# Optimization experiments

Hardware: AMD Instinct MI355X
Metric: run time of the kernel (lower is better)

The kernel has to match this reference:

```python
import jax, jax.numpy as jnp
import numpy as np

N = 50000          # nodes
F = 128            # feature dim (indim = outdim)
AVG_DEG = 12       # random edges per node (plus one self-loop)
AVG_D_LOG = 2.6    # avg_d['log'] used by PNA scalers
EPS = 1e-5         # PNA std epsilon / BatchNorm eps


def setup_inputs() -> dict:
    key = jax.random.key(0)
    k1, k2, k3, k4 = jax.random.split(key, 4)
    h = jax.random.normal(k1, (N, F), dtype=jnp.float32)
    E_rand = N * AVG_DEG
    src_r = jax.random.randint(k2, (E_rand,), 0, N)
    dst_r = jax.random.randint(k3, (E_rand,), 0, N)
    loop = jnp.arange(N)
    src = jnp.concatenate([src_r, loop]).astype(jnp.int64) if jax.config.jax_enable_x64 else jnp.concatenate([src_r, loop]).astype(jnp.int32)
    dst = jnp.concatenate([dst_r, loop]).astype(src.dtype)
    concat_dim = F * (1 + 4 * 3)  # indim * (1 + n_aggr * n_scalers)
    W = jax.random.normal(k4, (concat_dim, F), dtype=jnp.float32) * (1.0 / np.sqrt(concat_dim))
    b = jnp.zeros((F,), dtype=jnp.float32)
    gamma = jnp.ones((F,), dtype=jnp.float32)
    beta = jnp.zeros((F,), dtype=jnp.float32)
    return {"h": h, "src": src, "dst": dst, "W": W, "b": b, "gamma": gamma, "beta": beta}


def _pna_forward(h, W, b, gamma, beta, src, dst):
    n = h.shape[0]
    m = h[src]                                            # [E, F] gathered mailbox
    deg = jax.ops.segment_sum(jnp.ones(src.shape[0], h.dtype), dst, num_segments=n)
    deg = jnp.maximum(deg, 1.0)[:, None]                  # every node has a self-loop
    s = jax.ops.segment_sum(m, dst, num_segments=n)
    mean = s / deg
    mx = jax.ops.segment_max(m, dst, num_segments=n)
    mn = jax.ops.segment_min(m, dst, num_segments=n)
    mean_sq = jax.ops.segment_sum(m * m, dst, num_segments=n) / deg
    std = jnp.sqrt(jax.nn.relu(mean_sq - mean * mean) + EPS)
    agg = jnp.concatenate([mean, mx, mn, std], axis=1)    # [N, 4F]
    logd = jnp.log(deg + 1.0)                             # [N, 1]
    scaled = jnp.concatenate([agg,
                              agg * (logd / AVG_D_LOG),
                              agg * (AVG_D_LOG / logd)], axis=1)  # [N, 12F]
    hc = jnp.concatenate([h, scaled], axis=1)             # [N, 13F]
    out = hc @ W + b                                      # posttrans (single linear)
    out = jax.nn.relu(out)                                # activation (dropout p=0)
    mu = out.mean(axis=0)                                 # BatchNorm1d, training stats
    var = out.var(axis=0)                                 # biased variance (torch)
    out = gamma * (out - mu) * jax.lax.rsqrt(var + EPS) + beta
    return out


def reference(h, src, dst, W, b, gamma, beta):
    return _pna_forward(h, W, b, gamma, beta, src, dst)
```

## Files before the change

### kernel.cpp

```cpp
#include <hip/hip_runtime.h>
#include <math.h>

#define FDIM 128
#define AVG_D_LOGF 2.6f
#define BN_EPS 1e-5f
#define NK 10

using f32x2 = __attribute__((ext_vector_type(2))) float;
using f32x4 = __attribute__((ext_vector_type(4))) float;
using s16x8 = __attribute__((ext_vector_type(8))) short;
using u16x8 = __attribute__((ext_vector_type(8))) unsigned short;

__device__ __forceinline__ unsigned short f2bf(float x) {
  unsigned int u = __float_as_uint(x);
  u += 0x7FFFu + ((u >> 16) & 1u);
  return (unsigned short)(u >> 16);
}
__device__ __forceinline__ float bf2f(unsigned short u) {
  return __uint_as_float(((unsigned int)u) << 16);
}
__device__ __forceinline__ f32x2 bfpair(unsigned int u) {
  union { uint2 u2; f32x2 f; } c;
  c.u2 = make_uint2(u << 16, u & 0xFFFF0000u);
  return c.f;
}

__device__ __forceinline__ void gload16(const void* g, void* l) {
  __builtin_amdgcn_global_load_lds(
      (const __attribute__((address_space(1))) void*)g,
      (__attribute__((address_space(3))) void*)l, 16, 0, 0);
}

__global__ void prep_kernel(const float* __restrict__ h, unsigned short* __restrict__ hb,
                            const float* __restrict__ W, unsigned short* __restrict__ wBT,
                            const int* __restrict__ dst, int* __restrict__ deg,
                            int w0, int w1, int w2, int K) {
  int i = blockIdx.x * 256 + threadIdx.x;
  if (i < w0) {
    const f32x4* sp = (const f32x4*)h + (size_t)i * 2;
    f32x4 v0 = sp[0], v1 = sp[1];
    u16x8 o;
    o[0] = f2bf(v0[0]); o[1] = f2bf(v0[1]); o[2] = f2bf(v0[2]); o[3] = f2bf(v0[3]);
    o[4] = f2bf(v1[0]); o[5] = f2bf(v1[1]); o[6] = f2bf(v1[2]); o[7] = f2bf(v1[3]);
    *((u16x8*)hb + i) = o;
  } else if (i < w0 + w1) {
    int idx = i - w0;
    int k = idx >> 7, j = idx & 127;
    wBT[(size_t)j * K + k] = f2bf(W[idx]);
  } else if (i < w0 + w1 + w2) {
    atomicAdd(&deg[dst[i - w0 - w1]], 1);
  }
}

__global__ void scan1(const int* __restrict__ deg, int* __restrict__ offs,
                      int* __restrict__ bsums, int n) {
  __shared__ int tmp[256];
  int t = threadIdx.x, i = blockIdx.x * 256 + t;
  int v = (i < n) ? deg[i] : 0;
  tmp[t] = v; __syncthreads();
  for (int d = 1; d < 256; d <<= 1) {
    int x = (t >= d) ? tmp[t - d] : 0;
    __syncthreads();
    tmp[t] += x;
    __syncthreads();
  }
  if (i < n) offs[i] = tmp[t] - v;
  if (t == 255) bsums[blockIdx.x] = tmp[255];
}

__global__ void csr_fill(const int* __restrict__ src, const int* __restrict__ dst,
                         const int* __restrict__ offs, const int* __restrict__ bsums,
                         int* __restrict__ cursor, int* __restrict__ csr, int E, int nb) {
  __shared__ int tmp[256];
  __shared__ int ex[256];
  const int t = threadIdx.x;
  {
    int v = (t < nb) ? bsums[t] : 0;
    tmp[t] = v; __syncthreads();
    for (int d = 1; d < 256; d <<= 1) {
      int x = (t >= d) ? tmp[t - d] : 0;
      __syncthreads();
      tmp[t] += x;
      __syncthreads();
    }
    ex[t] = tmp[t] - v;
    __syncthreads();
  }
  int i = blockIdx.x * 256 + t;
  if (i < E) {
    int d = dst[i];
    int pos = offs[d] + ex[d >> 8] + atomicAdd(&cursor[d], 1);
    csr[pos] = src[i] << 8;
  }
}

__global__ __launch_bounds__(256) void agg_kernel(
    const unsigned short* __restrict__ hb, const int* __restrict__ csr,
    const int* __restrict__ offs, const int* __restrict__ bsums,
    unsigned short* __restrict__ aggb, float2* __restrict__ s12a,
    int n, int E, int nb) {
  __shared__ int tmp[256];
  __shared__ int ex[256];
  {
    int t = threadIdx.x;
    int v = (t < nb) ? bsums[t] : 0;
    tmp[t] = v; __syncthreads();
    for (int d = 1; d < 256; d <<= 1) {
      int x = (t >= d) ? tmp[t - d] : 0;
      __syncthreads();
      tmp[t] += x;
      __syncthreads();
    }
    ex[t] = tmp[t] - v;
    __syncthreads();
  }
  const int gw = (blockIdx.x * 256 + threadIdx.x) >> 6;
  const int lane = threadIdx.x & 63;
  if (gw >= n) return;
  const int beg = offs[gw] + ex[gw >> 8];
  const int end = (gw + 1 < n) ? offs[gw + 1] + ex[(gw + 1) >> 8] : E;
  const int sub = lane >> 5;
  const int fl  = lane & 31;
  const char* hbase = (const char*)hb + fl * 8;

  f32x2 s0v = {0.f, 0.f}, s1v = {0.f, 0.f};
  f32x2 q0v = {0.f, 0.f}, q1v = {0.f, 0.f};
  f32x2 mx0 = {-INFINITY, -INFINITY}, mx1 = {-INFINITY, -INFINITY};
  f32x2 mn0 = {INFINITY, INFINITY},  mn1 = {INFINITY, INFINITY};

  auto acc1 = [&](uint2 A) {
    f32x2 a0 = bfpair(A.x), a1 = bfpair(A.y);
    asm("v_pk_add_f32 %0, %0, %1" : "+v"(s0v) : "v"(a0));
    asm("v_pk_add_f32 %0, %0, %1" : "+v"(s1v) : "v"(a1));
    asm("v_pk_fma_f32 %0, %1, %1, %0" : "+v"(q0v) : "v"(a0));
    asm("v_pk_fma_f32 %0, %1, %1, %0" : "+v"(q1v) : "v"(a1));
    mx0[0] = fmaxf(mx0[0], a0[0]); mx0[1] = fmaxf(mx0[1], a0[1]);
    mx1[0] = fmaxf(mx1[0], a1[0]); mx1[1] = fmaxf(mx1[1], a1[1]);
    mn0[0] = fminf(mn0[0], a0[0]); mn0[1] = fminf(mn0[1], a0[1]);
    mn1[0] = fminf(mn1[0], a1[0]); mn1[1] = fminf(mn1[1], a1[1]);
  };
  auto gat = [&](int byteoff) -> uint2 {
    return *(const uint2*)(hbase + byteoff);
  };

  const int cnt = end - beg;
  const int pairs = cnt >> 1;
  int p = 0;
  for (; p + 4 <= pairs; p += 4) {
    int base = beg + 2 * p + sub;
    int i0 = csr[base], i1 = csr[base + 2], i2 = csr[base + 4], i3 = csr[base + 6];
    uint2 A = gat(i0), B = gat(i1), C = gat(i2), D = gat(i3);
    acc1(A); acc1(B); acc1(C); acc1(D);
  }
  for (; p < pairs; ++p) {
    acc1(gat(csr[beg + 2 * p + sub]));
  }
  if ((cnt & 1) && sub == 0) {
    acc1(gat(csr[end - 1]));
  }

  s0v[0] += __shfl_xor(s0v[0], 32); s0v[1] += __shfl_xor(s0v[1], 32);
  s1v[0] += __shfl_xor(s1v[0], 32); s1v[1] += __shfl_xor(s1v[1], 32);
  q0v[0] += __shfl_xor(q0v[0], 32); q0v[1] += __shfl_xor(q0v[1], 32);
  q1v[0] += __shfl_xor(q1v[0], 32); q1v[1] += __shfl_xor(q1v[1], 32);
  mx0[0] = fmaxf(mx0[0], __shfl_xor(mx0[0], 32)); mx0[1] = fmaxf(mx0[1], __shfl_xor(mx0[1], 32));
  mx1[0] = fmaxf(mx1[0], __shfl_xor(mx1[0], 32)); mx1[1] = fmaxf(mx1[1], __shfl_xor(mx1[1], 32));
  mn0[0] = fminf(mn0[0], __shfl_xor(mn0[0], 32)); mn0[1] = fminf(mn0[1], __shfl_xor(mn0[1], 32));
  mn1[0] = fminf(mn1[0], __shfl_xor(mn1[0], 32)); mn1[1] = fminf(mn1[1], __shfl_xor(mn1[1], 32));

  float degf = (float)cnt;
  if (degf < 1.f) degf = 1.f;
  const float inv = 1.f / degf;
  if (sub == 0) {
    float me0 = s0v[0] * inv, me1 = s0v[1] * inv, me2 = s1v[0] * inv, me3 = s1v[1] * inv;
    float st0 = sqrtf(fmaxf(q0v[0] * inv - me0 * me0, 0.f) + BN_EPS);
    float st1 = sqrtf(fmaxf(q0v[1] * inv - me1 * me1, 0.f) + BN_EPS);
    float st2 = sqrtf(fmaxf(q1v[0] * inv - me2 * me2, 0.f) + BN_EPS);
    float st3 = sqrtf(fmaxf(q1v[1] * inv - me3 * me3, 0.f) + BN_EPS);
    unsigned int b = (unsigned int)gw * 512u + (unsigned int)fl * 4u;
    uint2 wme = make_uint2((unsigned int)f2bf(me0) | ((unsigned int)f2bf(me1) << 16),
                           (unsigned int)f2bf(me2) | ((unsigned int)f2bf(me3) << 16));
    uint2 wmx = make_uint2((unsigned int)f2bf(mx0[0]) | ((unsigned int)f2bf(mx0[1]) << 16),
                           (unsigned int)f2bf(mx1[0]) | ((unsigned int)f2bf(mx1[1]) << 16));
    uint2 wmn = make_uint2((unsigned int)f2bf(mn0[0]) | ((unsigned int)f2bf(mn0[1]) << 16),
                           (unsigned int)f2bf(mn1[0]) | ((unsigned int)f2bf(mn1[1]) << 16));
    uint2 wst = make_uint2((unsigned int)f2bf(st0) | ((unsigned int)f2bf(st1) << 16),
                           (unsigned int)f2bf(st2) | ((unsigned int)f2bf(st3) << 16));
    *(uint2*)&aggb[b      ] = wme;
    *(uint2*)&aggb[b + 128] = wmx;
    *(uint2*)&aggb[b + 256] = wmn;
    *(uint2*)&aggb[b + 384] = wst;
  }
  if (lane == 0) {
    float logd = logf(degf + 1.f);
    s12a[gw] = make_float2(logd / AVG_D_LOGF, AVG_D_LOGF / logd);
  }
}

__global__ __launch_bounds__(256, 2) void gemm_kernel(
    const unsigned short* __restrict__ hb, const unsigned short* __restrict__ wBT,
    const unsigned short* __restrict__ aggb, const float2* __restrict__ s12a,
    const float* __restrict__ bias, float* __restrict__ out,
    float* __restrict__ bnsum, float* __restrict__ bnsq, int n, int K) {
  __shared__ s16x8 AsB[2][1024];
  __shared__ s16x8 BsB[2][3][512];
  const int t = threadIdx.x;
  const int lane = t & 63;
  const int w = t >> 6;
  const int wr = w >> 1, wc = w & 1;
  const int hi = lane >> 4, lr = lane & 15, rx7 = lr & 7;

  const int nwg = gridDim.x;
  const int q = nwg >> 3, r = nwg & 7;
  const int xcd = blockIdx.x & 7, jj = blockIdx.x >> 3;
  const int bx = (xcd < r ? xcd * (q + 1) : r * (q + 1) + (xcd - r) * q) + jj;

  const int m0 = (bx >> 1) * 128;
  const int n0 = (bx & 1) * 64;

  f32x4 acc[3][4][2] = {};

  auto stage = [&](int ss, int buf) {
    const bool ph1 = (ss < 2);
    #pragma unroll
    for (int i = 0; i < 4; ++i) {
      int unit = w * 256 + i * 64 + lane;
      int row = unit >> 3, x = unit & 7;
      int node = m0 + row; if (node >= n) node = n - 1;
      int xo = (x ^ (row & 7)) << 3;
      const unsigned short* src = ph1
          ? hb   + (size_t)node * FDIM + ss * 64 + xo
          : aggb + (size_t)node * 512 + (ss - 2) * 64 + xo;
      gload16(src, &AsB[buf][w * 256 + i * 64]);
    }
    const int nsec = ph1 ? 1 : 3;
    for (int s = 0; s < nsec; ++s) {
      int koff = ph1 ? ss * 64 : (FDIM + s * 512 + (ss - 2) * 64);
      #pragma unroll
      for (int i = 0; i < 2; ++i) {
        int unit = w * 128 + i * 64 + lane;
        int row = unit >> 3, x = unit & 7;
        const unsigned short* src =
            wBT + (size_t)(n0 + row) * K + koff + ((x ^ (row & 7)) << 3);
        gload16(src, &BsB[buf][s][w * 128 + i * 64]);
      }
    }
  };

  stage(0, 0);
  int cur = 0;
  for (int step = 0; step < NK; ++step) {
    if (step + 1 < NK) {
      stage(step + 1, cur ^ 1);
      if (step + 1 < 2) asm volatile("s_waitcnt vmcnt(6)" ::: "memory");
      else              asm volatile("s_waitcnt vmcnt(10)" ::: "memory");
    } else {
      asm volatile("s_waitcnt vmcnt(0)" ::: "memory");
    }
    asm volatile("s_barrier" ::: "memory");
    #pragma unroll
    for (int ks = 0; ks < 2; ++ks) {
      s16x8 a[4];
      #pragma unroll
      for (int m = 0; m < 4; ++m) {
        int row = wr * 64 + m * 16 + lr;
        a[m] = AsB[cur][row * 8 + ((ks * 4 + hi) ^ rx7)];
      }
      #pragma unroll
      for (int s = 0; s < 3; ++s) {
        if (step < 2 && s > 0) continue;
        int rb = wc * 32 + lr;
        s16x8 b0 = BsB[cur][s][rb * 8 + ((ks * 4 + hi) ^ rx7)];
        s16x8 b1 = BsB[cur][s][(rb + 16) * 8 + ((ks * 4 + hi) ^ rx7)];
        #pragma unroll
        for (int m = 0; m < 4; ++m) {
          acc[s][m][0] = __builtin_amdgcn_mfma_f32_16x16x32_bf16(a[m], b0, acc[s][m][0], 0, 0, 0);
          acc[s][m][1] = __builtin_amdgcn_mfma_f32_16x16x32_bf16(a[m], b1, acc[s][m][1], 0, 0, 0);
        }
      }
    }
    asm volatile("s_barrier" ::: "memory");
    cur ^= 1;
  }

  float* red = (float*)&AsB[0][0];
  if (t < 128) red[t] = 0.f;
  __syncthreads();

  const float bv0 = bias[n0 + wc * 32 + lr];
  const float bv1 = bias[n0 + wc * 32 + 16 + lr];
  float cs[2] = {0.f, 0.f}, cq[2] = {0.f, 0.f};
  #pragma unroll
  for (int m = 0; m < 4; ++m) {
    #pragma unroll
    for (int i = 0; i < 4; ++i) {
      int grow = m0 + wr * 64 + m * 16 + hi * 4 + i;
      if (grow >= n) continue;
      float2 sv = s12a[grow];
      #pragma unroll
      for (int nn = 0; nn < 2; ++nn) {
        float v = acc[0][m][nn][i] + sv.x * acc[1][m][nn][i] + sv.y * acc[2][m][nn][i]
                + (nn ? bv1 : bv0);
        v = fmaxf(v, 0.f);
        out[(size_t)grow * FDIM + n0 + wc * 32 + nn * 16 + lr] = v;
        cs[nn] += v; cq[nn] += v * v;
      }
    }
  }
  #pragma unroll
  for (int nn = 0; nn < 2; ++nn) {
    int lc = wc * 32 + nn * 16 + lr;
    atomicAdd(&red[lc], cs[nn]);
    atomicAdd(&red[64 + lc], cq[nn]);
  }
  __syncthreads();
  if (t < 64)       atomicAdd(&bnsum[n0 + t], red[t]);
  else if (t < 128) atomicAdd(&bnsq[n0 + t - 64], red[t]);
}

__global__ void bn_norm(float* __restrict__ out, const float* __restrict__ bnsum,
                        const float* __restrict__ bnsq, const float* __restrict__ gamma,
                        const float* __restrict__ beta, int n) {
  __shared__ float scs[128], shs[128];
  const int t = threadIdx.x;
  if (t < 128) {
    const float invN = 1.f / (float)n;
    const float mu = bnsum[t] * invN;
    const float var = bnsq[t] * invN - mu * mu;
    const float rs = rsqrtf(var + BN_EPS);
    const float s = gamma[t] * rs;
    scs[t] = s; shs[t] = beta[t] - mu * s;
  }
  __syncthreads();
  const int total = n * 32;
  int idx = blockIdx.x * 256 + t;
  const int c4 = (idx & 31) * 4;
  const float s0 = scs[c4], s1 = scs[c4 + 1], s2 = scs[c4 + 2], s3 = scs[c4 + 3];
  const float h0 = shs[c4], h1 = shs[c4 + 1], h2 = shs[c4 + 2], h3 = shs[c4 + 3];
  for (; idx < total; idx += gridDim.x * 256) {
    f32x4 v = ((f32x4*)out)[idx];
    v[0] = v[0] * s0 + h0;
    v[1] = v[1] * s1 + h1;
    v[2] = v[2] * s2 + h2;
    v[3] = v[3] * s3 + h3;
    ((f32x4*)out)[idx] = v;
  }
}

extern "C" void kernel_launch(void* const* d_in, const int* in_sizes, int n_in,
                              void* d_out, int out_size, void* d_ws, size_t ws_size,
                              hipStream_t stream) {
  const float* h     = (const float*)d_in[0];
  const int*   src   = (const int*)d_in[1];
  const int*   dst   = (const int*)d_in[2];
  const float* W     = (const float*)d_in[3];
  const float* bias  = (const float*)d_in[4];
  const float* gamma = (const float*)d_in[5];
  const float* beta  = (const float*)d_in[6];
  float* out = (float*)d_out;

  const int n = in_sizes[0] / FDIM;
  const int E = in_sizes[1];
  const int K = in_sizes[3] / FDIM;

  char* base = (char*)d_ws;
  size_t off = 0;
  auto alloc = [&](size_t bytes) -> void* {
    void* p = base + off;
    off += (bytes + 255) & ~(size_t)255;
    return p;
  };
  int*   deg    = (int*)  alloc(4ull * n);
  int*   cursor = (int*)  alloc(4ull * n);
  float* bnsum  = (float*)alloc(512);
  float* bnsq   = (float*)alloc(512);
  const size_t zlen = off;
  int*    offs  = (int*)  alloc(4ull * (n + 1));
  int*    bsums = (int*)  alloc(4ull * 256);
  int*    csr   = (int*)  alloc(4ull * E);
  float2* s12a  = (float2*)alloc(8ull * n);
  unsigned short* aggb = (unsigned short*)alloc(2ull * (size_t)n * 512);
  unsigned short* wBT  = (unsigned short*)alloc(2ull * (size_t)K * FDIM);
  unsigned short* hb   = (unsigned short*)alloc(2ull * (size_t)n * FDIM);
  (void)ws_size; (void)n_in; (void)out_size;

  const int eb = (E + 255) / 256;
  const int nb = (n + 255) / 256;
  const int w0 = n * FDIM / 8;
  const int w1 = K * FDIM;
  const int w2 = E;

  hipMemsetAsync(d_ws, 0, zlen, stream);
  prep_kernel<<<(w0 + w1 + w2 + 255) / 256, 256, 0, stream>>>(h, hb, W, wBT, dst, deg,
                                                              w0, w1, w2, K);
  scan1<<<nb, 256, 0, stream>>>(deg, offs, bsums, n);
  csr_fill<<<eb, 256, 0, stream>>>(src, dst, offs, bsums, cursor, csr, E, nb);
  agg_kernel<<<(n + 3) / 4, 256, 0, stream>>>(hb, csr, offs, bsums, aggb, s12a, n, E, nb);
  const int gblocks = ((n + 127) / 128) * 2;
  gemm_kernel<<<gblocks, 256, 0, stream>>>(hb, wBT, aggb, s12a, bias,
                                           out, bnsum, bnsq, n, K);
  bn_norm<<<2048, 256, 0, stream>>>(out, bnsum, bnsq, gamma, beta, n);
}
```

Measured before the change: 175.1 us.

## Replace double-buffered K=64 GEMM pipeline with single-buffered K=128 steps

The GEMM main loop now stages 128-wide K slices in five steps instead of 64-wide slices in ten. It drops the double buffer and the manual vmcnt waits in favour of __syncthreads, so global-to-LDS loads no longer overlap MFMA work. Fewer iterations and barriers are traded for lost load/compute overlap, with LDS size unchanged. The aggregation kernel's inline-asm packed add/fma is also replaced with plain vector arithmetic, leaving instruction choice to the compiler.

```diff
diff --git a/kernel.cpp b/kernel.cpp
--- a/kernel.cpp
+++ b/kernel.cpp
@@ -4,7 +4,7 @@
 #define FDIM 128
 #define AVG_D_LOGF 2.6f
 #define BN_EPS 1e-5f
-#define NK 10
+#define NK5 5
 
 using f32x2 = __attribute__((ext_vector_type(2))) float;
 using f32x4 = __attribute__((ext_vector_type(4))) float;
@@ -16,15 +16,11 @@
   u += 0x7FFFu + ((u >> 16) & 1u);
   return (unsigned short)(u >> 16);
 }
-__device__ __forceinline__ float bf2f(unsigned short u) {
-  return __uint_as_float(((unsigned int)u) << 16);
-}
 __device__ __forceinline__ f32x2 bfpair(unsigned int u) {
   union { uint2 u2; f32x2 f; } c;
   c.u2 = make_uint2(u << 16, u & 0xFFFF0000u);
   return c.f;
 }
-
 __device__ __forceinline__ void gload16(const void* g, void* l) {
   __builtin_amdgcn_global_load_lds(
       (const __attribute__((address_space(1))) void*)g,
@@ -130,10 +126,8 @@
 
   auto acc1 = [&](uint2 A) {
     f32x2 a0 = bfpair(A.x), a1 = bfpair(A.y);
-    asm("v_pk_add_f32 %0, %0, %1" : "+v"(s0v) : "v"(a0));
-    asm("v_pk_add_f32 %0, %0, %1" : "+v"(s1v) : "v"(a1));
-    asm("v_pk_fma_f32 %0, %1, %1, %0" : "+v"(q0v) : "v"(a0));
-    asm("v_pk_fma_f32 %0, %1, %1, %0" : "+v"(q1v) : "v"(a1));
+    s0v += a0; s1v += a1;
+    q0v += a0 * a0; q1v += a1 * a1;
     mx0[0] = fmaxf(mx0[0], a0[0]); mx0[1] = fmaxf(mx0[1], a0[1]);
     mx1[0] = fmaxf(mx1[0], a1[0]); mx1[1] = fmaxf(mx1[1], a1[1]);
     mn0[0] = fminf(mn0[0], a0[0]); mn0[1] = fminf(mn0[1], a0[1]);
@@ -202,8 +196,8 @@
     const unsigned short* __restrict__ aggb, const float2* __restrict__ s12a,
     const float* __restrict__ bias, float* __restrict__ out,
     float* __restrict__ bnsum, float* __restrict__ bnsq, int n, int K) {
-  __shared__ s16x8 AsB[2][1024];
-  __shared__ s16x8 BsB[2][3][512];
+  __shared__ s16x8 As[2048];
+  __shared__ s16x8 Bs[3][1024];
   const int t = threadIdx.x;
   const int lane = t & 63;
   const int w = t >> 6;
@@ -220,58 +214,53 @@
 
   f32x4 acc[3][4][2] = {};
 
-  auto stage = [&](int ss, int buf) {
-    const bool ph1 = (ss < 2);
+  auto stage = [&](int ss) {
+    const bool ph1 = (ss == 0);
     #pragma unroll
-    for (int i = 0; i < 4; ++i) {
-      int unit = w * 256 + i * 64 + lane;
-      int row = unit >> 3, x = unit & 7;
+    for (int i = 0; i < 8; ++i) {
+      int unit = w * 512 + i * 64 + lane;
+      int row = unit >> 4, xf = unit & 15;
+      int half = xf >> 3, x = xf & 7;
       int node = m0 + row; if (node >= n) node = n - 1;
-      int xo = (x ^ (row & 7)) << 3;
+      int col = half * 64 + ((x ^ (row & 7)) << 3);
       const unsigned short* src = ph1
-          ? hb   + (size_t)node * FDIM + ss * 64 + xo
-          : aggb + (size_t)node * 512 + (ss - 2) * 64 + xo;
-      gload16(src, &AsB[buf][w * 256 + i * 64]);
+          ? hb   + (size_t)node * FDIM + col
+          : aggb + (size_t)node * 512 + (ss - 1) * 128 + col;
+      gload16(src, &As[w * 512 + i * 64]);
     }
     const int nsec = ph1 ? 1 : 3;
     for (int s = 0; s < nsec; ++s) {
-      int koff = ph1 ? ss * 64 : (FDIM + s * 512 + (ss - 2) * 64);
+      int koff = ph1 ? 0 : (FDIM + s * 512 + (ss - 1) * 128);
       #pragma unroll
-      for (int i = 0; i < 2; ++i) {
-        int unit = w * 128 + i * 64 + lane;
-        int row = unit >> 3, x = unit & 7;
-        const unsigned short* src =
-            wBT + (size_t)(n0 + row) * K + koff + ((x ^ (row & 7)) << 3);
-        gload16(src, &BsB[buf][s][w * 128 + i * 64]);
+      for (int i = 0; i < 4; ++i) {
+        int unit = w * 256 + i * 64 + lane;
+        int row = unit >> 4, xf = unit & 15;
+        int half = xf >> 3, x = xf & 7;
+        int col = half * 64 + ((x ^ (row & 7)) << 3);
+        const unsigned short* src = wBT + (size_t)(n0 + row) * K + koff + col;
+        gload16(src, &Bs[s][w * 256 + i * 64]);
       }
     }
   };
 
-  stage(0, 0);
-  int cur = 0;
-  for (int step = 0; step < NK; ++step) {
-    if (step + 1 < NK) {
-      stage(step + 1, cur ^ 1);
-      if (step + 1 < 2) asm volatile("s_waitcnt vmcnt(6)" ::: "memory");
-      else              asm volatile("s_waitcnt vmcnt(10)" ::: "memory");
-    } else {
-      asm volatile("s_waitcnt vmcnt(0)" ::: "memory");
-    }
-    asm volatile("s_barrier" ::: "memory");
+  for (int step = 0; step < NK5; ++step) {
+    stage(step);
+    __syncthreads();
     #pragma unroll
-    for (int ks = 0; ks < 2; ++ks) {
+    for (int ks = 0; ks < 4; ++ks) {
+      const int uidx = ((ks >> 1) << 3) + ((((ks << 2) + hi) & 7) ^ rx7);
       s16x8 a[4];
       #pragma unroll
       for (int m = 0; m < 4; ++m) {
         int row = wr * 64 + m * 16 + lr;
-        a[m] = AsB[cur][row * 8 + ((ks * 4 + hi) ^ rx7)];
+        a[m] = As[row * 16 + uidx];
       }
       #pragma unroll
       for (int s = 0; s < 3; ++s) {
-        if (step < 2 && s > 0) continue;
+        if (step == 0 && s > 0) continue;
         int rb = wc * 32 + lr;
-        s16x8 b0 = BsB[cur][s][rb * 8 + ((ks * 4 + hi) ^ rx7)];
-        s16x8 b1 = BsB[cur][s][(rb + 16) * 8 + ((ks * 4 + hi) ^ rx7)];
+        s16x8 b0 = Bs[s][rb * 16 + uidx];
+        s16x8 b1 = Bs[s][(rb + 16) * 16 + uidx];
         #pragma unroll
         for (int m = 0; m < 4; ++m) {
           acc[s][m][0] = __builtin_amdgcn_mfma_f32_16x16x32_bf16(a[m], b0, acc[s][m][0], 0, 0, 0);
@@ -279,11 +268,10 @@
         }
       }
     }
-    asm volatile("s_barrier" ::: "memory");
-    cur ^= 1;
-  }
-
-  float* red = (float*)&AsB[0][0];
+    __syncthreads();
+  }
+
+  float* red = (float*)&As[0];
   if (t < 128) red[t] = 0.f;
   __syncthreads();
 
```

Result: no change. 174.5 us (-0.3%).

## Prefetch aggregate A-tiles through registers two stages ahead in GEMM loop

Applied to the files above, without the earlier changes.

Restructures the fused GEMM main loop. The two h-phase steps now run unpipelined with direct LDS loads. The aggregate-phase A tiles are loaded into registers two k-steps ahead and written to LDS after compute, while B tiles still use async global-to-LDS loads one step ahead. Address computation is hoisted out of the staging lambdas, and the loop is fully unrolled with hand-tuned vmcnt waits. This aims to hide more global-load latency for the large aggregate operand, at the cost of extra registers, fragile manual waitcount bookkeeping and a non-overlapped first phase. The aggregation kernel's inline-asm packed ops are also replaced with plain vector arithmetic.

```diff
diff --git a/kernel.cpp b/kernel.cpp
--- a/kernel.cpp
+++ b/kernel.cpp
@@ -4,7 +4,6 @@
 #define FDIM 128
 #define AVG_D_LOGF 2.6f
 #define BN_EPS 1e-5f
-#define NK 10
 
 using f32x2 = __attribute__((ext_vector_type(2))) float;
 using f32x4 = __attribute__((ext_vector_type(4))) float;
@@ -16,15 +15,11 @@
   u += 0x7FFFu + ((u >> 16) & 1u);
   return (unsigned short)(u >> 16);
 }
-__device__ __forceinline__ float bf2f(unsigned short u) {
-  return __uint_as_float(((unsigned int)u) << 16);
-}
 __device__ __forceinline__ f32x2 bfpair(unsigned int u) {
   union { uint2 u2; f32x2 f; } c;
   c.u2 = make_uint2(u << 16, u & 0xFFFF0000u);
   return c.f;
 }
-
 __device__ __forceinline__ void gload16(const void* g, void* l) {
   __builtin_amdgcn_global_load_lds(
       (const __attribute__((address_space(1))) void*)g,
@@ -130,10 +125,8 @@
 
   auto acc1 = [&](uint2 A) {
     f32x2 a0 = bfpair(A.x), a1 = bfpair(A.y);
-    asm("v_pk_add_f32 %0, %0, %1" : "+v"(s0v) : "v"(a0));
-    asm("v_pk_add_f32 %0, %0, %1" : "+v"(s1v) : "v"(a1));
-    asm("v_pk_fma_f32 %0, %1, %1, %0" : "+v"(q0v) : "v"(a0));
-    asm("v_pk_fma_f32 %0, %1, %1, %0" : "+v"(q1v) : "v"(a1));
+    s0v += a0; s1v += a1;
+    q0v += a0 * a0; q1v += a1 * a1;
     mx0[0] = fmaxf(mx0[0], a0[0]); mx0[1] = fmaxf(mx0[1], a0[1]);
     mx1[0] = fmaxf(mx1[0], a1[0]); mx1[1] = fmaxf(mx1[1], a1[1]);
     mn0[0] = fminf(mn0[0], a0[0]); mn0[1] = fminf(mn0[1], a0[1]);
@@ -152,12 +145,8 @@
     uint2 A = gat(i0), B = gat(i1), C = gat(i2), D = gat(i3);
     acc1(A); acc1(B); acc1(C); acc1(D);
   }
-  for (; p < pairs; ++p) {
-    acc1(gat(csr[beg + 2 * p + sub]));
-  }
-  if ((cnt & 1) && sub == 0) {
-    acc1(gat(csr[end - 1]));
-  }
+  for (; p < pairs; ++p) acc1(gat(csr[beg + 2 * p + sub]));
+  if ((cnt & 1) && sub == 0) acc1(gat(csr[end - 1]));
 
   s0v[0] += __shfl_xor(s0v[0], 32); s0v[1] += __shfl_xor(s0v[1], 32);
   s1v[0] += __shfl_xor(s1v[0], 32); s1v[1] += __shfl_xor(s1v[1], 32);
@@ -220,52 +209,53 @@
 
   f32x4 acc[3][4][2] = {};
 
-  auto stage = [&](int ss, int buf) {
+  const unsigned short* aH[4];
+  const unsigned short* aG[4];
+  #pragma unroll
+  for (int i = 0; i < 4; ++i) {
+    int unit = w * 256 + i * 64 + lane;
+    int row = unit >> 3, x = unit & 7;
+    int node = m0 + row; if (node >= n) node = n - 1;
+    int col = (x ^ (row & 7)) << 3;
+    aH[i] = hb   + (size_t)node * FDIM + col;
+    aG[i] = aggb + (size_t)node * 512  + col;
+  }
+  const unsigned short* bB[2];
+  #pragma unroll
+  for (int i = 0; i < 2; ++i) {
+    int unit = w * 128 + i * 64 + lane;
+    int row = unit >> 3, x = unit & 7;
+    bB[i] = wBT + (size_t)(n0 + row) * K + ((x ^ (row & 7)) << 3);
+  }
+
+  auto stageB = [&](int ss, int buf) {
     const bool ph1 = (ss < 2);
-    #pragma unroll
-    for (int i = 0; i < 4; ++i) {
-      int unit = w * 256 + i * 64 + lane;
-      int row = unit >> 3, x = unit & 7;
-      int node = m0 + row; if (node >= n) node = n - 1;
-      int xo = (x ^ (row & 7)) << 3;
-      const unsigned short* src = ph1
-          ? hb   + (size_t)node * FDIM + ss * 64 + xo
-          : aggb + (size_t)node * 512 + (ss - 2) * 64 + xo;
-      gload16(src, &AsB[buf][w * 256 + i * 64]);
-    }
     const int nsec = ph1 ? 1 : 3;
     for (int s = 0; s < nsec; ++s) {
       int koff = ph1 ? ss * 64 : (FDIM + s * 512 + (ss - 2) * 64);
       #pragma unroll
-      for (int i = 0; i < 2; ++i) {
-        int unit = w * 128 + i * 64 + lane;
-        int row = unit >> 3, x = unit & 7;
-        const unsigned short* src =
-            wBT + (size_t)(n0 + row) * K + koff + ((x ^ (row & 7)) << 3);
-        gload16(src, &BsB[buf][s][w * 128 + i * 64]);
-      }
-    }
-  };
-
-  stage(0, 0);
-  int cur = 0;
-  for (int step = 0; step < NK; ++step) {
-    if (step + 1 < NK) {
-      stage(step + 1, cur ^ 1);
-      if (step + 1 < 2) asm volatile("s_waitcnt vmcnt(6)" ::: "memory");
-      else              asm volatile("s_waitcnt vmcnt(10)" ::: "memory");
-    } else {
-      asm volatile("s_waitcnt vmcnt(0)" ::: "memory");
-    }
-    asm volatile("s_barrier" ::: "memory");
+      for (int i = 0; i < 2; ++i)
+        gload16(bB[i] + koff, &BsB[buf][s][w * 128 + i * 64]);
+    }
+  };
+  s16x8 rA[4], rA2[4];
+  auto loadA = [&](int ss, s16x8* rr) {
+    #pragma unroll
+    for (int i = 0; i < 4; ++i)
+      rr[i] = *(const s16x8*)(aG[i] + (ss - 2) * 64);
+  };
+  auto writeA = [&](const s16x8* rr, int buf) {
+    #pragma unroll
+    for (int i = 0; i < 4; ++i)
+      AsB[buf][w * 256 + i * 64 + lane] = rr[i];
+  };
+  auto compute = [&](int step, int cur) {
     #pragma unroll
     for (int ks = 0; ks < 2; ++ks) {
       s16x8 a[4];
       #pragma unroll
-      for (int m = 0; m < 4; ++m) {
-        int row = wr * 64 + m * 16 + lr;
-        a[m] = AsB[cur][row * 8 + ((ks * 4 + hi) ^ rx7)];
-      }
+      for (int m = 0; m < 4; ++m)
+        a[m] = AsB[cur][(wr * 64 + m * 16 + lr) * 8 + ((ks * 4 + hi) ^ rx7)];
       #pragma unroll
       for (int s = 0; s < 3; ++s) {
         if (step < 2 && s > 0) continue;
@@ -279,11 +269,52 @@
         }
       }
     }
-    asm volatile("s_barrier" ::: "memory");
-    cur ^= 1;
+  };
+
+  #pragma unroll
+  for (int ss = 0; ss < 2; ++ss) {
+    #pragma unroll
+    for (int i = 0; i < 4; ++i)
+      gload16(aH[i] + ss * 64, &AsB[ss][w * 256 + i * 64]);
+    stageB(ss, ss);
+    __syncthreads();
+    compute(0, ss);
+    __syncthreads();
+  }
+
+  stageB(2, 0);
+  asm volatile("" ::: "memory");
+  loadA(2, rA);
+  asm volatile("s_waitcnt vmcnt(0)" ::: "memory");
+  writeA(rA, 0);
+  loadA(3, rA);
+  asm volatile("s_waitcnt lgkmcnt(0)" ::: "memory");
+  __builtin_amdgcn_s_barrier();
+
+  #pragma unroll
+  for (int tt = 2; tt <= 9; ++tt) {
+    const int p = tt & 1;
+    if (tt <= 8) {
+      stageB(tt + 1, p ^ 1);
+      asm volatile("" ::: "memory");
+    }
+    if (tt <= 7) loadA(tt + 2, rA2);
+    compute(2, p);
+    if (tt <= 8) {
+      if (tt <= 7) asm volatile("s_waitcnt vmcnt(10)" ::: "memory");
+      else         asm volatile("s_waitcnt vmcnt(6)"  ::: "memory");
+      writeA(rA, p ^ 1);
+      #pragma unroll
+      for (int i = 0; i < 4; ++i) rA[i] = rA2[i];
+      if (tt <= 7) asm volatile("s_waitcnt vmcnt(4)" ::: "memory");
+      else         asm volatile("s_waitcnt vmcnt(0)" ::: "memory");
+      asm volatile("s_waitcnt lgkmcnt(0)" ::: "memory");
+      __builtin_amdgcn_s_barrier();
+    }
   }
 
   float* red = (float*)&AsB[0][0];
+  __syncthreads();
   if (t < 128) red[t] = 0.f;
   __syncthreads();
 
```

Result: no change. 177.3 us (+1.3%).

## Shrink GEMM M-tile to 64 rows, drop double buffering, raise occupancy

Applied to the files above, without the earlier changes.

The GEMM block tile is halved from 128 to 64 rows, so the grid doubles and each wave holds half as many accumulators. The double-buffered async LDS pipeline with manual vmcnt waits is replaced by a single buffer loaded then synchronized with __syncthreads, and launch bounds are raised to allow 4 blocks per CU. The agg kernel's inline-asm packed add/fma is replaced with vector-type arithmetic the compiler may lower equivalently. The aim is more blocks in flight to hide latency, at the cost of losing intra-block load/compute overlap and more redundant B-tile loads.

```diff
diff --git a/kernel.cpp b/kernel.cpp
--- a/kernel.cpp
+++ b/kernel.cpp
@@ -16,15 +16,11 @@
   u += 0x7FFFu + ((u >> 16) & 1u);
   return (unsigned short)(u >> 16);
 }
-__device__ __forceinline__ float bf2f(unsigned short u) {
-  return __uint_as_float(((unsigned int)u) << 16);
-}
 __device__ __forceinline__ f32x2 bfpair(unsigned int u) {
   union { uint2 u2; f32x2 f; } c;
   c.u2 = make_uint2(u << 16, u & 0xFFFF0000u);
   return c.f;
 }
-
 __device__ __forceinline__ void gload16(const void* g, void* l) {
   __builtin_amdgcn_global_load_lds(
       (const __attribute__((address_space(1))) void*)g,
@@ -130,10 +126,8 @@
 
   auto acc1 = [&](uint2 A) {
     f32x2 a0 = bfpair(A.x), a1 = bfpair(A.y);
-    asm("v_pk_add_f32 %0, %0, %1" : "+v"(s0v) : "v"(a0));
-    asm("v_pk_add_f32 %0, %0, %1" : "+v"(s1v) : "v"(a1));
-    asm("v_pk_fma_f32 %0, %1, %1, %0" : "+v"(q0v) : "v"(a0));
-    asm("v_pk_fma_f32 %0, %1, %1, %0" : "+v"(q1v) : "v"(a1));
+    s0v += a0; s1v += a1;
+    q0v += a0 * a0; q1v += a1 * a1;
     mx0[0] = fmaxf(mx0[0], a0[0]); mx0[1] = fmaxf(mx0[1], a0[1]);
     mx1[0] = fmaxf(mx1[0], a1[0]); mx1[1] = fmaxf(mx1[1], a1[1]);
     mn0[0] = fminf(mn0[0], a0[0]); mn0[1] = fminf(mn0[1], a0[1]);
@@ -152,12 +146,8 @@
     uint2 A = gat(i0), B = gat(i1), C = gat(i2), D = gat(i3);
     acc1(A); acc1(B); acc1(C); acc1(D);
   }
-  for (; p < pairs; ++p) {
-    acc1(gat(csr[beg + 2 * p + sub]));
-  }
-  if ((cnt & 1) && sub == 0) {
-    acc1(gat(csr[end - 1]));
-  }
+  for (; p < pairs; ++p) acc1(gat(csr[beg + 2 * p + sub]));
+  if ((cnt & 1) && sub == 0) acc1(gat(csr[end - 1]));
 
   s0v[0] += __shfl_xor(s0v[0], 32); s0v[1] += __shfl_xor(s0v[1], 32);
   s1v[0] += __shfl_xor(s1v[0], 32); s1v[1] += __shfl_xor(s1v[1], 32);
@@ -197,13 +187,13 @@
   }
 }
 
-__global__ __launch_bounds__(256, 2) void gemm_kernel(
+__global__ __launch_bounds__(256, 4) void gemm_kernel(
     const unsigned short* __restrict__ hb, const unsigned short* __restrict__ wBT,
     const unsigned short* __restrict__ aggb, const float2* __restrict__ s12a,
     const float* __restrict__ bias, float* __restrict__ out,
     float* __restrict__ bnsum, float* __restrict__ bnsq, int n, int K) {
-  __shared__ s16x8 AsB[2][1024];
-  __shared__ s16x8 BsB[2][3][512];
+  __shared__ s16x8 As[512];
+  __shared__ s16x8 Bs[3][512];
   const int t = threadIdx.x;
   const int lane = t & 63;
   const int w = t >> 6;
@@ -215,23 +205,23 @@
   const int xcd = blockIdx.x & 7, jj = blockIdx.x >> 3;
   const int bx = (xcd < r ? xcd * (q + 1) : r * (q + 1) + (xcd - r) * q) + jj;
 
-  const int m0 = (bx >> 1) * 128;
+  const int m0 = (bx >> 1) * 64;
   const int n0 = (bx & 1) * 64;
 
-  f32x4 acc[3][4][2] = {};
-
-  auto stage = [&](int ss, int buf) {
+  f32x4 acc[3][2][2] = {};
+
+  auto stage = [&](int ss) {
     const bool ph1 = (ss < 2);
     #pragma unroll
-    for (int i = 0; i < 4; ++i) {
-      int unit = w * 256 + i * 64 + lane;
+    for (int i = 0; i < 2; ++i) {
+      int unit = w * 128 + i * 64 + lane;
       int row = unit >> 3, x = unit & 7;
       int node = m0 + row; if (node >= n) node = n - 1;
       int xo = (x ^ (row & 7)) << 3;
       const unsigned short* src = ph1
           ? hb   + (size_t)node * FDIM + ss * 64 + xo
           : aggb + (size_t)node * 512 + (ss - 2) * 64 + xo;
-      gload16(src, &AsB[buf][w * 256 + i * 64]);
+      gload16(src, &As[w * 128 + i * 64]);
     }
     const int nsec = ph1 ? 1 : 3;
     for (int s = 0; s < nsec; ++s) {
@@ -242,48 +232,40 @@
         int row = unit >> 3, x = unit & 7;
         const unsigned short* src =
             wBT + (size_t)(n0 + row) * K + koff + ((x ^ (row & 7)) << 3);
-        gload16(src, &BsB[buf][s][w * 128 + i * 64]);
+        gload16(src, &Bs[s][w * 128 + i * 64]);
       }
     }
   };
 
-  stage(0, 0);
-  int cur = 0;
   for (int step = 0; step < NK; ++step) {
-    if (step + 1 < NK) {
-      stage(step + 1, cur ^ 1);
-      if (step + 1 < 2) asm volatile("s_waitcnt vmcnt(6)" ::: "memory");
-      else              asm volatile("s_waitcnt vmcnt(10)" ::: "memory");
-    } else {
-      asm volatile("s_waitcnt vmcnt(0)" ::: "memory");
-    }
-    asm volatile("s_barrier" ::: "memory");
+    stage(step);
+    __syncthreads();
     #pragma unroll
     for (int ks = 0; ks < 2; ++ks) {
-      s16x8 a[4];
+      const int uo = (ks * 4 + hi);
+      s16x8 a[2];
       #pragma unroll
-      for (int m = 0; m < 4; ++m) {
-        int row = wr * 64 + m * 16 + lr;
-        a[m] = AsB[cur][row * 8 + ((ks * 4 + hi) ^ rx7)];
+      for (int m = 0; m < 2; ++m) {
+        int row = wr * 32 + m * 16 + lr;
+        a[m] = As[row * 8 + ((uo & 7) ^ rx7)];
       }
       #pragma unroll
       for (int s = 0; s < 3; ++s) {
         if (step < 2 && s > 0) continue;
         int rb = wc * 32 + lr;
-        s16x8 b0 = BsB[cur][s][rb * 8 + ((ks * 4 + hi) ^ rx7)];
-        s16x8 b1 = BsB[cur][s][(rb + 16) * 8 + ((ks * 4 + hi) ^ rx7)];
+        s16x8 b0 = Bs[s][rb * 8 + ((uo & 7) ^ rx7)];
+        s16x8 b1 = Bs[s][(rb + 16) * 8 + ((uo & 7) ^ rx7)];
         #pragma unroll
-        for (int m = 0; m < 4; ++m) {
+        for (int m = 0; m < 2; ++m) {
           acc[s][m][0] = __builtin_amdgcn_mfma_f32_16x16x32_bf16(a[m], b0, acc[s][m][0], 0, 0, 0);
           acc[s][m][1] = __builtin_amdgcn_mfma_f32_16x16x32_bf16(a[m], b1, acc[s][m][1], 0, 0, 0);
         }
       }
     }
-    asm volatile("s_barrier" ::: "memory");
-    cur ^= 1;
-  }
-
-  float* red = (float*)&AsB[0][0];
+    __syncthreads();
+  }
+
+  float* red = (float*)&As[0];
   if (t < 128) red[t] = 0.f;
   __syncthreads();
 
@@ -291,10 +273,10 @@
   const float bv1 = bias[n0 + wc * 32 + 16 + lr];
   float cs[2] = {0.f, 0.f}, cq[2] = {0.f, 0.f};
   #pragma unroll
-  for (int m = 0; m < 4; ++m) {
+  for (int m = 0; m < 2; ++m) {
     #pragma unroll
     for (int i = 0; i < 4; ++i) {
-      int grow = m0 + wr * 64 + m * 16 + hi * 4 + i;
+      int grow = m0 + wr * 32 + m * 16 + hi * 4 + i;
       if (grow >= n) continue;
       float2 sv = s12a[grow];
       #pragma unroll
@@ -396,7 +378,7 @@
   scan1<<<nb, 256, 0, stream>>>(deg, offs, bsums, n);
   csr_fill<<<eb, 256, 0, stream>>>(src, dst, offs, bsums, cursor, csr, E, nb);
   agg_kernel<<<(n + 3) / 4, 256, 0, stream>>>(hb, csr, offs, bsums, aggb, s12a, n, E, nb);
-  const int gblocks = ((n + 127) / 128) * 2;
+  const int gblocks = ((n + 63) / 64) * 2;
   gemm_kernel<<<gblocks, 256, 0, stream>>>(hb, wBT, aggb, s12a, bias,
                                            out, bnsum, bnsq, n, K);
   bn_norm<<<2048, 256, 0, stream>>>(out, bnsum, bnsq, gamma, beta, n);
```

Result: slower. 179.9 us (+2.7%).
